# Kernel tuning notes

Measured on AMD Instinct MI355X. Metric: run time of the kernel, lower is better.

## Reference

```python
import jax, jax.numpy as jnp
import numpy as np
import math

V, D, H, FF, L, S, B = 32000, 1024, 16, 4096, 8, 1024, 4
HD = D // H


def _pos_encoding(seq_len, dim):
    pos = np.arange(seq_len)[:, None].astype(np.float32)
    div = np.exp(np.arange(0, dim, 2).astype(np.float32) * -(math.log(10000.0) / dim))
    pe = np.zeros((seq_len, dim), dtype=np.float32)
    pe[:, 0::2] = np.sin(pos * div)
    pe[:, 1::2] = np.cos(pos * div)
    return jnp.asarray(pe)


def setup_inputs() -> dict:
    key = jax.random.key(0)
    ks = jax.random.split(key, 24)
    sc = 0.02
    inp = {
        'tokens': jax.random.randint(ks[0], (B, S), 0, V),
        'emb_W': jax.random.normal(ks[1], (V, D), jnp.float32) * sc,
        'Wq': jax.random.normal(ks[2], (L, D, D), jnp.float32) * sc,
        'bq': jnp.zeros((L, D), jnp.float32),
        'Wk': jax.random.normal(ks[3], (L, D, D), jnp.float32) * sc,
        'bk': jnp.zeros((L, D), jnp.float32),
        'Wv': jax.random.normal(ks[4], (L, D, D), jnp.float32) * sc,
        'bv': jnp.zeros((L, D), jnp.float32),
        'Wo': jax.random.normal(ks[5], (L, D, D), jnp.float32) * sc,
        'bo': jnp.zeros((L, D), jnp.float32),
        'ln1_g': jnp.ones((L, D), jnp.float32),
        'ln1_b': jnp.zeros((L, D), jnp.float32),
        'ln2_g': jnp.ones((L, D), jnp.float32),
        'ln2_b': jnp.zeros((L, D), jnp.float32),
        'W1': jax.random.normal(ks[6], (L, D, FF), jnp.float32) * sc,
        'b1': jnp.zeros((L, FF), jnp.float32),
        'W2': jax.random.normal(ks[7], (L, FF, D), jnp.float32) * sc,
        'b2': jnp.zeros((L, D), jnp.float32),
        'lnf_g': jnp.ones((D,), jnp.float32),
        'lnf_b': jnp.zeros((D,), jnp.float32),
        'head_W': jax.random.normal(ks[8], (D, V), jnp.float32) * sc,
        'head_b': jnp.zeros((V,), jnp.float32),
    }
    return inp


def _layernorm(x, g, b, eps=1e-5):
    mu = jnp.mean(x, axis=-1, keepdims=True)
    var = jnp.mean(jnp.square(x - mu), axis=-1, keepdims=True)
    return (x - mu) * jax.lax.rsqrt(var + eps) * g + b


def _attention(x, Wq, bq, Wk, bk, Wv, bv, Wo, bo, causal_mask):
    b, s, d = x.shape
    q = (x @ Wq + bq).reshape(b, s, H, HD).transpose(0, 2, 1, 3)
    k = (x @ Wk + bk).reshape(b, s, H, HD).transpose(0, 2, 1, 3)
    v = (x @ Wv + bv).reshape(b, s, H, HD).transpose(0, 2, 1, 3)
    scores = jnp.einsum('bhqd,bhkd->bhqk', q, k) / math.sqrt(HD)
    scores = jnp.where(causal_mask, scores, -1e9)
    attn = jax.nn.softmax(scores, axis=-1)
    out = jnp.einsum('bhqk,bhkd->bhqd', attn, v)
    out = out.transpose(0, 2, 1, 3).reshape(b, s, d)
    return out @ Wo + bo


def reference(tokens, emb_W, Wq, bq, Wk, bk, Wv, bv, Wo, bo,
              ln1_g, ln1_b, ln2_g, ln2_b, W1, b1, W2, b2,
              lnf_g, lnf_b, head_W, head_b):
    b, s = tokens.shape
    mask = jnp.tril(jnp.ones((s, s), bool))[None, None]  # (1,1,s,s)
    x = emb_W[tokens] + _pos_encoding(s, D)[None]
    for l in range(L):
        a = _attention(_layernorm(x, ln1_g[l], ln1_b[l]),
                       Wq[l], bq[l], Wk[l], bk[l], Wv[l], bv[l], Wo[l], bo[l], mask)
        x = x + a
        h = _layernorm(x, ln2_g[l], ln2_b[l])
        h = jax.nn.relu(h @ W1[l] + b1[l]) @ W2[l] + b2[l]
        x = x + h
    x = _layernorm(x, lnf_g, lnf_b)
    return x @ head_W + head_b
```

## Files before the change

kernel.cpp:

```cpp
#include <hip/hip_runtime.h>
#include <math.h>


using u16 = unsigned short;
using u32 = unsigned int;
typedef __attribute__((ext_vector_type(4))) float  f32x4;
typedef __attribute__((ext_vector_type(8))) short  s16x8;
typedef __attribute__((ext_vector_type(8))) __bf16 bf16x8;

__device__ __forceinline__ u16 f2bf(float f) {
  u32 u = __builtin_bit_cast(u32, f);
  u += 0x7fffu + ((u >> 16) & 1u);
  return (u16)(u >> 16);
}

__device__ __forceinline__ f32x4 mfma16(s16x8 a, s16x8 b, f32x4 c) {
  return __builtin_amdgcn_mfma_f32_16x16x32_bf16(
      __builtin_bit_cast(bf16x8, a), __builtin_bit_cast(bf16x8, b), c, 0, 0, 0);
}

#define GLD16(gp, lp) __builtin_amdgcn_global_load_lds(                    \
    (const __attribute__((address_space(1))) void*)(gp),                   \
    (__attribute__((address_space(3))) void*)(lp), 16, 0, 0)

__global__ __launch_bounds__(256) void transpose_cvt(
    const float* __restrict__ in, u16* __restrict__ out,
    int C, long long inLS, long long outLS, int outRS)
{
  __shared__ float t[32][33];
  int tr = threadIdx.x >> 5, tc = threadIdx.x & 31;
  const float* ip = in + (size_t)blockIdx.z * inLS +
                    ((size_t)blockIdx.x * 32 + tr) * C + blockIdx.y * 32 + tc;
#pragma unroll
  for (int p = 0; p < 4; ++p) t[p * 8 + tr][tc] = ip[(size_t)p * 8 * C];
  __syncthreads();
  u16* op = out + (size_t)blockIdx.z * outLS +
            ((size_t)blockIdx.y * 32 + tr) * outRS + (size_t)blockIdx.x * 32 + tc;
#pragma unroll
  for (int p = 0; p < 4; ++p) op[(size_t)p * 8 * outRS] = f2bf(t[tc][p * 8 + tr]);
}

__global__ __launch_bounds__(256) void pack_bqkv(
    const float* __restrict__ bq, const float* __restrict__ bk,
    const float* __restrict__ bv, float* __restrict__ outb)
{
  int i = blockIdx.x * 256 + threadIdx.x;
  int ly = i / 3072, j = i % 3072;
  float v = (j < 1024) ? bq[ly * 1024 + j]
          : (j < 2048) ? bk[ly * 1024 + (j - 1024)]
                       : bv[ly * 1024 + (j - 2048)];
  outb[i] = v;
}

__global__ __launch_bounds__(256) void embed_kernel(
    const int* __restrict__ tokens, const float* __restrict__ embW,
    float* __restrict__ x)
{
  int row = blockIdx.x;
  int s = row & 1023;
  int tok = tokens[row];
  int d0 = threadIdx.x * 4;
  float4 e = *(const float4*)&embW[(size_t)tok * 1024 + d0];
  const float c = -9.210340371976184f / 1024.0f;
  float div0 = expf((float)d0 * c);
  float div1 = expf((float)(d0 + 2) * c);
  float sn0, cs0, sn1, cs1;
  sincosf((float)s * div0, &sn0, &cs0);
  sincosf((float)s * div1, &sn1, &cs1);
  float4 r;
  r.x = e.x + sn0; r.y = e.y + cs0; r.z = e.z + sn1; r.w = e.w + cs1;
  *(float4*)&x[(size_t)row * 1024 + d0] = r;
}

__global__ __launch_bounds__(256) void ln_kernel(
    const float* __restrict__ x, const float* __restrict__ g,
    const float* __restrict__ b, u16* __restrict__ y)
{
  int row = blockIdx.x, tid = threadIdx.x;
  float4 v = *(const float4*)&x[(size_t)row * 1024 + tid * 4];
  float sum = v.x + v.y + v.z + v.w;
  float sq = v.x * v.x + v.y * v.y + v.z * v.z + v.w * v.w;
#pragma unroll
  for (int o = 32; o > 0; o >>= 1) {
    sum += __shfl_xor(sum, o, 64);
    sq  += __shfl_xor(sq,  o, 64);
  }
  __shared__ float ps[8];
  int w = tid >> 6;
  if ((tid & 63) == 0) { ps[w] = sum; ps[4 + w] = sq; }
  __syncthreads();
  sum = ps[0] + ps[1] + ps[2] + ps[3];
  sq  = ps[4] + ps[5] + ps[6] + ps[7];
  float mu = sum * (1.0f / 1024.0f);
  float var = sq * (1.0f / 1024.0f) - mu * mu;
  float rs = rsqrtf(var + 1e-5f);
  float4 gg = *(const float4*)&g[tid * 4];
  float4 bb = *(const float4*)&b[tid * 4];
  u32 lo = (u32)f2bf((v.x - mu) * rs * gg.x + bb.x) |
           ((u32)f2bf((v.y - mu) * rs * gg.y + bb.y) << 16);
  u32 hi = (u32)f2bf((v.z - mu) * rs * gg.z + bb.z) |
           ((u32)f2bf((v.w - mu) * rs * gg.w + bb.w) << 16);
  uint2 o2; o2.x = lo; o2.y = hi;
  *(uint2*)&y[(size_t)row * 1024 + tid * 4] = o2;
}

template<int OMODE, int RELU, int NT>
__global__ __launch_bounds__(512, 2) void gemm256(
    const u16* __restrict__ A, const u16* __restrict__ Bt,
    const float* __restrict__ bias, void* Cp, int M, int N, int K, int gx)
{
  __shared__ alignas(16) u16 lds[2][16384];
  const int tid = threadIdx.x;
  const int w = tid >> 6, l = tid & 63;
  const int g = l >> 4, lr = l & 15;
  const int wm = w >> 2, wn = w & 3;
  int nwg = gridDim.x;
  int bid = blockIdx.x;
  int swz = (bid & 7) * (nwg >> 3) + (bid >> 3);
  int bx = swz % gx, by = swz / gx;
  int m0 = by << 8, n0 = bx << 8;

  const u16* Ag[2]; const u16* Bg[2]; int dstE[2];
#pragma unroll
  for (int s2 = 0; s2 < 2; ++s2) {
    int idx = s2 * 512 + tid;
    int row = idx >> 2;
    int ch = (idx & 3) ^ ((row >> 1) & 3);
    Ag[s2] = A  + (size_t)(m0 + row) * K + ch * 8;
    Bg[s2] = Bt + (size_t)(n0 + row) * K + ch * 8;
    dstE[s2] = idx * 8;
  }
  const int colx = (g ^ ((lr >> 1) & 3)) * 8;
  const int aoff = (wm * 128 + lr) * 32 + colx;
  const int boff = 8192 + (wn * 64 + lr) * 32 + colx;

  f32x4 acc[8][4];
#pragma unroll
  for (int i = 0; i < 8; ++i)
#pragma unroll
    for (int j = 0; j < 4; ++j) acc[i][j] = f32x4{0.f, 0.f, 0.f, 0.f};

  const int nk = K >> 5;
#pragma unroll
  for (int s2 = 0; s2 < 2; ++s2) GLD16(Ag[s2], &lds[0][dstE[s2]]);
#pragma unroll
  for (int s2 = 0; s2 < 2; ++s2) GLD16(Bg[s2], &lds[0][8192 + dstE[s2]]);
  asm volatile("s_waitcnt vmcnt(0)" ::: "memory");
  __builtin_amdgcn_s_barrier();

  int cur = 0;
  s16x8 aC[4], aH[4], bC[4];
#pragma unroll
  for (int i = 0; i < 4; ++i) aC[i] = *(const s16x8*)&lds[0][aoff + i * 512];
#pragma unroll
  for (int i = 0; i < 4; ++i) aH[i] = *(const s16x8*)&lds[0][aoff + (4 + i) * 512];
#pragma unroll
  for (int j = 0; j < 4; ++j) bC[j] = *(const s16x8*)&lds[0][boff + j * 512];

  for (int t = 0; t < nk; ++t) {
    const bool more = (t + 1 < nk);
    if (more) {
      const int kn = (t + 1) << 5;
#pragma unroll
      for (int s2 = 0; s2 < 2; ++s2) GLD16(Ag[s2] + kn, &lds[cur ^ 1][dstE[s2]]);
#pragma unroll
      for (int s2 = 0; s2 < 2; ++s2) GLD16(Bg[s2] + kn, &lds[cur ^ 1][8192 + dstE[s2]]);
    }
    __builtin_amdgcn_s_setprio(1);
#pragma unroll
    for (int i = 0; i < 4; ++i)
#pragma unroll
      for (int j = 0; j < 4; ++j) acc[i][j] = mfma16(aC[i], bC[j], acc[i][j]);
#pragma unroll
    for (int i = 0; i < 4; ++i)
#pragma unroll
      for (int j = 0; j < 4; ++j) acc[4 + i][j] = mfma16(aH[i], bC[j], acc[4 + i][j]);
    __builtin_amdgcn_s_setprio(0);
    if (more) {
      asm volatile("s_waitcnt vmcnt(0)" ::: "memory");
      __builtin_amdgcn_s_barrier();
      cur ^= 1;
#pragma unroll
      for (int i = 0; i < 4; ++i) aC[i] = *(const s16x8*)&lds[cur][aoff + i * 512];
#pragma unroll
      for (int i = 0; i < 4; ++i) aH[i] = *(const s16x8*)&lds[cur][aoff + (4 + i) * 512];
#pragma unroll
      for (int j = 0; j < 4; ++j) bC[j] = *(const s16x8*)&lds[cur][boff + j * 512];
    }
  }

  float* fst = (float*)(void*)&lds[0][0];
#pragma unroll
  for (int mf = 0; mf < 8; ++mf) {
    __builtin_amdgcn_s_barrier();
#pragma unroll
    for (int nf = 0; nf < 4; ++nf) {
      int cl = wn * 64 + nf * 16 + lr;
      float bv = bias[n0 + cl];
      int rl = wm * 16 + g * 4;
#pragma unroll
      for (int r = 0; r < 4; ++r) {
        float v = acc[mf][nf][r] + bv;
        if (RELU) v = fmaxf(v, 0.f);
        fst[(rl + r) * 260 + cl] = v;
      }
    }
    __builtin_amdgcn_s_barrier();
    if (OMODE == 0) {
#pragma unroll
      for (int it = 0; it < 2; ++it) {
        int seg = it * 512 + tid;
        int row = seg >> 5;
        int co  = (seg & 31) * 8;
        int grow = m0 + (row >> 4) * 128 + mf * 16 + (row & 15);
        const float* src = &fst[row * 260 + co];
        uint4 q;
        q.x = (u32)f2bf(src[0]) | ((u32)f2bf(src[1]) << 16);
        q.y = (u32)f2bf(src[2]) | ((u32)f2bf(src[3]) << 16);
        q.z = (u32)f2bf(src[4]) | ((u32)f2bf(src[5]) << 16);
        q.w = (u32)f2bf(src[6]) | ((u32)f2bf(src[7]) << 16);
        *(uint4*)&((u16*)Cp)[(size_t)grow * N + n0 + co] = q;
      }
    } else {
#pragma unroll
      for (int it = 0; it < 4; ++it) {
        int seg = it * 512 + tid;
        int row = seg >> 6;
        int co  = (seg & 63) * 4;
        int grow = m0 + (row >> 4) * 128 + mf * 16 + (row & 15);
        f32x4 q = *(const f32x4*)&fst[row * 260 + co];
        float* dp = &((float*)Cp)[(size_t)grow * N + n0 + co];
        if (NT) __builtin_nontemporal_store(q, (f32x4*)dp);
        else    *(f32x4*)dp = q;
      }
    }
  }
}

template<int OMODE, int RELU>
__global__ __launch_bounds__(256, 3) void gemm_p(
    const u16* __restrict__ A, const u16* __restrict__ Bt,
    const float* __restrict__ bias, const float* res, void* Cp,
    int M, int N, int K, int gx)
{
  __shared__ alignas(16) u16 lds[2][8192];
  const int tid = threadIdx.x;
  const int w = tid >> 6, l = tid & 63;
  const int g = l >> 4, lr = l & 15;
  const int wm = w >> 1, wn = w & 1;
  int nwg = gridDim.x;
  int bid = blockIdx.x;
  int swz = (bid & 7) * (nwg >> 3) + (bid >> 3);
  int bx = swz % gx, by = swz / gx;
  int m0 = by << 7, n0 = bx << 7;

  const u16 *Ag[2], *Bg[2];
  int dstA[2], dstB[2];
#pragma unroll
  for (int s = 0; s < 2; ++s) {
    int idx = s * 256 + tid;
    int row = idx >> 2;
    int ch = (idx & 3) ^ ((row >> 1) & 3);
    Ag[s] = A  + (size_t)(m0 + row) * K + ch * 8;
    Bg[s] = Bt + (size_t)(n0 + row) * K + ch * 8;
    dstA[s] = idx * 8;
    dstB[s] = 4096 + idx * 8;
  }
  const int colx = (g ^ ((lr >> 1) & 3)) * 8;
  const int aoff = (wm * 64 + lr) * 32 + colx;
  const int boff = 4096 + (wn * 64 + lr) * 32 + colx;

  f32x4 acc[4][4];
#pragma unroll
  for (int i = 0; i < 4; ++i)
#pragma unroll
    for (int j = 0; j < 4; ++j) acc[i][j] = f32x4{0.f, 0.f, 0.f, 0.f};

  const int nk = K >> 5;
#pragma unroll
  for (int s = 0; s < 2; ++s) GLD16(Ag[s], &lds[0][dstA[s]]);
#pragma unroll
  for (int s = 0; s < 2; ++s) GLD16(Bg[s], &lds[0][dstB[s]]);
  asm volatile("s_waitcnt vmcnt(0)" ::: "memory");
  __builtin_amdgcn_s_barrier();

  int cur = 0;
  s16x8 aC[4], bC[4];
#pragma unroll
  for (int i = 0; i < 4; ++i) aC[i] = *(const s16x8*)&lds[0][aoff + i * 512];
#pragma unroll
  for (int j = 0; j < 4; ++j) bC[j] = *(const s16x8*)&lds[0][boff + j * 512];

  for (int t = 0; t < nk; ++t) {
    const bool more = (t + 1 < nk);
    if (more) {
      const int kn = (t + 1) << 5;
#pragma unroll
      for (int s = 0; s < 2; ++s) GLD16(Ag[s] + kn, &lds[cur ^ 1][dstA[s]]);
#pragma unroll
      for (int s = 0; s < 2; ++s) GLD16(Bg[s] + kn, &lds[cur ^ 1][dstB[s]]);
    }
    __builtin_amdgcn_s_setprio(1);
#pragma unroll
    for (int i = 0; i < 4; ++i)
#pragma unroll
      for (int j = 0; j < 4; ++j) acc[i][j] = mfma16(aC[i], bC[j], acc[i][j]);
    __builtin_amdgcn_s_setprio(0);
    if (more) {
      asm volatile("s_waitcnt vmcnt(0)" ::: "memory");
      __builtin_amdgcn_s_barrier();
      cur ^= 1;
#pragma unroll
      for (int i = 0; i < 4; ++i) aC[i] = *(const s16x8*)&lds[cur][aoff + i * 512];
#pragma unroll
      for (int j = 0; j < 4; ++j) bC[j] = *(const s16x8*)&lds[cur][boff + j * 512];
    }
  }
#pragma unroll
  for (int mf = 0; mf < 4; ++mf) {
    int row = m0 + wm * 64 + mf * 16 + g * 4;
#pragma unroll
    for (int nf = 0; nf < 4; ++nf) {
      int col = n0 + wn * 64 + nf * 16 + lr;
      float bv = bias[col];
#pragma unroll
      for (int r = 0; r < 4; ++r) {
        float v = acc[mf][nf][r] + bv;
        if (RELU) v = fmaxf(v, 0.f);
        size_t idx = (size_t)(row + r) * N + col;
        if (OMODE == 0)      ((u16*)Cp)[idx] = f2bf(v);
        else if (OMODE == 1) ((float*)Cp)[idx] = v + res[idx];
        else                 ((float*)Cp)[idx] = v;
      }
    }
  }
}

__global__ __launch_bounds__(256) void attn_kernel(
    const u16* __restrict__ qkv, u16* __restrict__ outp)
{
  int b = blockIdx.x >> 4, h = blockIdx.x & 15;
  int q0 = blockIdx.y << 6;
  int tid = threadIdx.x, w = tid >> 6, l = tid & 63;
  int g = l >> 4, lr = l & 15;
  const int RS = 3072;
  const u16* base = qkv + (size_t)b * 1024 * RS + h * 64;
  const u16* Qb = base;
  const u16* Kb = base + 1024;
  const u16* Vb = base + 2048;
  __shared__ alignas(16) u16 Plds[4][1024];
  __shared__ alignas(16) u16 Vt[4096];
  char* Pw = (char*)&Plds[w][0];

  s16x8 qf[2];
#pragma unroll
  for (int ks = 0; ks < 2; ++ks)
    qf[ks] = *(const s16x8*)&Qb[(size_t)(q0 + w * 16 + lr) * RS + ks * 32 + g * 8];

  f32x4 o[4];
#pragma unroll
  for (int n = 0; n < 4; ++n) o[n] = f32x4{0.f, 0.f, 0.f, 0.f};
  float mr[4] = {-INFINITY, -INFINITY, -INFINITY, -INFINITY};
  float ls[4] = {0.f, 0.f, 0.f, 0.f};

  int ntile = (q0 >> 6) + 1;
  for (int kt = 0; kt < ntile; ++kt) {
    int kv0 = kt << 6;
    f32x4 sc[4];
#pragma unroll
    for (int t = 0; t < 4; ++t) sc[t] = f32x4{0.f, 0.f, 0.f, 0.f};
#pragma unroll
    for (int ks = 0; ks < 2; ++ks)
#pragma unroll
      for (int t = 0; t < 4; ++t) {
        s16x8 kf = *(const s16x8*)&Kb[(size_t)(kv0 + t * 16 + lr) * RS + ks * 32 + g * 8];
        sc[t] = mfma16(qf[ks], kf, sc[t]);
      }
#pragma unroll
    for (int p = 0; p < 2; ++p) {
      int key = p * 32 + (tid >> 3);
      int d0 = (tid & 7) * 8;
      s16x8 vrow = *(const s16x8*)&Vb[(size_t)(kv0 + key) * RS + d0];
#pragma unroll
      for (int j = 0; j < 8; ++j) {
        int d = d0 + j;
        int byt = (d * 128 + key * 2) ^ ((d & 7) << 4);
        *(u16*)((char*)Vt + byt) = (u16)vrow[j];
      }
    }
    float p4[4][4];
    float tmax[4] = {-INFINITY, -INFINITY, -INFINITY, -INFINITY};
    int qr_base = q0 + w * 16 + g * 4;
#pragma unroll
    for (int t = 0; t < 4; ++t) {
      int key = kv0 + t * 16 + lr;
#pragma unroll
      for (int r = 0; r < 4; ++r) {
        float s = sc[t][r] * 0.125f;
        s = (key <= qr_base + r) ? s : -1e30f;
        p4[t][r] = s;
        tmax[r] = fmaxf(tmax[r], s);
      }
    }
#pragma unroll
    for (int off = 1; off < 16; off <<= 1)
#pragma unroll
      for (int r = 0; r < 4; ++r) tmax[r] = fmaxf(tmax[r], __shfl_xor(tmax[r], off, 64));
    float corr[4], rsum[4];
#pragma unroll
    for (int r = 0; r < 4; ++r) {
      float mn = fmaxf(mr[r], tmax[r]);
      corr[r] = __expf(mr[r] - mn);
      mr[r] = mn;
      rsum[r] = 0.f;
    }
#pragma unroll
    for (int t = 0; t < 4; ++t)
#pragma unroll
      for (int r = 0; r < 4; ++r) {
        float e = __expf(p4[t][r] - mr[r]);
        p4[t][r] = e;
        rsum[r] += e;
      }
#pragma unroll
    for (int off = 1; off < 16; off <<= 1)
#pragma unroll
      for (int r = 0; r < 4; ++r) rsum[r] += __shfl_xor(rsum[r], off, 64);
#pragma unroll
    for (int r = 0; r < 4; ++r) ls[r] = ls[r] * corr[r] + rsum[r];
#pragma unroll
    for (int n = 0; n < 4; ++n)
#pragma unroll
      for (int r = 0; r < 4; ++r) o[n][r] *= corr[r];
#pragma unroll
    for (int t = 0; t < 4; ++t)
#pragma unroll
      for (int r = 0; r < 4; ++r) {
        int prow = g * 4 + r;
        int byt = (prow * 128 + (t * 16 + lr) * 2) ^ ((prow & 7) << 4);
        *(u16*)(Pw + byt) = f2bf(p4[t][r]);
      }
    __syncthreads();
#pragma unroll
    for (int ks = 0; ks < 2; ++ks) {
      int ab = (lr * 128 + ks * 64 + g * 16) ^ ((lr & 7) << 4);
      s16x8 pa = *(const s16x8*)(Pw + ab);
#pragma unroll
      for (int n = 0; n < 4; ++n) {
        int vb2 = ((n * 16 + lr) * 128 + ks * 64 + g * 16) ^ ((lr & 7) << 4);
        s16x8 vfr = *(const s16x8*)((const char*)Vt + vb2);
        o[n] = mfma16(pa, vfr, o[n]);
      }
    }
    __syncthreads();
  }
#pragma unroll
  for (int n = 0; n < 4; ++n)
#pragma unroll
    for (int r = 0; r < 4; ++r) {
      float v = o[n][r] / ls[r];
      outp[(size_t)(b * 1024 + q0 + w * 16 + g * 4 + r) * 1024 + h * 64 + n * 16 + lr] = f2bf(v);
    }
}

extern "C" void kernel_launch(void* const* d_in, const int* in_sizes, int n_in,
                              void* d_out, int out_size, void* d_ws, size_t ws_size,
                              hipStream_t stream)
{
  const int*   tokens = (const int*)  d_in[0];
  const float* embW   = (const float*)d_in[1];
  const float* Wq     = (const float*)d_in[2];
  const float* bq     = (const float*)d_in[3];
  const float* Wk     = (const float*)d_in[4];
  const float* bk     = (const float*)d_in[5];
  const float* Wv     = (const float*)d_in[6];
  const float* bv     = (const float*)d_in[7];
  const float* Wo     = (const float*)d_in[8];
  const float* bo     = (const float*)d_in[9];
  const float* ln1g   = (const float*)d_in[10];
  const float* ln1b   = (const float*)d_in[11];
  const float* ln2g   = (const float*)d_in[12];
  const float* ln2b   = (const float*)d_in[13];
  const float* W1     = (const float*)d_in[14];
  const float* b1     = (const float*)d_in[15];
  const float* W2     = (const float*)d_in[16];
  const float* b2     = (const float*)d_in[17];
  const float* lnfg   = (const float*)d_in[18];
  const float* lnfb   = (const float*)d_in[19];
  const float* headW  = (const float*)d_in[20];
  const float* headb  = (const float*)d_in[21];
  (void)in_sizes; (void)n_in; (void)out_size;

  char* ws = (char*)d_ws;
  u16*   qkvT = (u16*)(ws);
  u16*   woT  = (u16*)(ws + 50331648);
  u16*   w1T  = (u16*)(ws + 67108864);
  u16*   w2T  = (u16*)(ws + 134217728);
  u16*   headT= (u16*)(ws + 201326592);
  float* bqkv = (float*)(ws + 266862592);
  float* x    = (float*)(ws + 266960896);
  u16*   y    = (u16*)(ws + 283738112);
  u16*   qkv  = (u16*)(ws + 292126720);
  u16*   attno= (u16*)(ws + 317292544);
  u16*   h1   = (u16*)(ws + 325681152);
  if (ws_size < 359235584ull) return;

  dim3 blk(256);
  dim3 blk5(512);
  transpose_cvt<<<dim3(32, 32, 8),  blk, 0, stream>>>(Wq, qkvT,           1024,  1048576LL, 3145728LL, 1024);
  transpose_cvt<<<dim3(32, 32, 8),  blk, 0, stream>>>(Wk, qkvT + 1048576, 1024,  1048576LL, 3145728LL, 1024);
  transpose_cvt<<<dim3(32, 32, 8),  blk, 0, stream>>>(Wv, qkvT + 2097152, 1024,  1048576LL, 3145728LL, 1024);
  transpose_cvt<<<dim3(32, 32, 8),  blk, 0, stream>>>(Wo, woT,            1024,  1048576LL, 1048576LL, 1024);
  transpose_cvt<<<dim3(32, 128, 8), blk, 0, stream>>>(W1, w1T,            4096,  4194304LL, 4194304LL, 1024);
  transpose_cvt<<<dim3(128, 32, 8), blk, 0, stream>>>(W2, w2T,            1024,  4194304LL, 4194304LL, 4096);
  transpose_cvt<<<dim3(32, 1000, 1),blk, 0, stream>>>(headW, headT,       32000, 0LL,       0LL,       1024);
  pack_bqkv<<<96, blk, 0, stream>>>(bq, bk, bv, bqkv);
  embed_kernel<<<4096, blk, 0, stream>>>(tokens, embW, x);
  for (int ly = 0; ly < 8; ++ly) {
    ln_kernel<<<4096, blk, 0, stream>>>(x, ln1g + ly * 1024, ln1b + ly * 1024, y);
    gemm256<0, 0, 0><<<192, blk5, 0, stream>>>(y, qkvT + (size_t)ly * 3145728,
        bqkv + ly * 3072, qkv, 4096, 3072, 1024, 12);
    attn_kernel<<<dim3(64, 16), blk, 0, stream>>>(qkv, attno);
    gemm_p<1, 0><<<256, blk, 0, stream>>>(attno, woT + (size_t)ly * 1048576,
        bo + ly * 1024, x, x, 4096, 1024, 1024, 8);
    ln_kernel<<<4096, blk, 0, stream>>>(x, ln2g + ly * 1024, ln2b + ly * 1024, y);
    gemm256<0, 1, 0><<<256, blk5, 0, stream>>>(y, w1T + (size_t)ly * 4194304,
        b1 + ly * 4096, h1, 4096, 4096, 1024, 16);
    gemm_p<1, 0><<<256, blk, 0, stream>>>(h1, w2T + (size_t)ly * 4194304,
        b2 + ly * 1024, x, x, 4096, 1024, 4096, 8);
  }
  ln_kernel<<<4096, blk, 0, stream>>>(x, lnfg, lnfb, y);
  gemm256<2, 0, 1><<<2000, blk5, 0, stream>>>(y, headT, headb,
      (float*)d_out, 4096, 32000, 1024, 125);
}
```

Before: 2.776 ms.

## Double GEMM K-tile to 64, re-swizzle LDS, add M-major tile ordering for head

The 256x256 GEMM now stages 64-wide K slices, using an 8-chunk XOR swizzle, and loads all fragments from LDS at the start of each iteration. This halves the number of barriers per K. A template flag selects M-major block ordering, which the LM-head GEMM uses so that weight tiles get reused across M. Nontemporal stores are removed. The LDS footprint doubles to 128KB, which likely limits residency to one block per CU and removes the register prefetch overlap.

```diff
diff --git a/kernel.cpp b/kernel.cpp
--- a/kernel.cpp
+++ b/kernel.cpp
@@ -104,12 +104,12 @@
   *(uint2*)&y[(size_t)row * 1024 + tid * 4] = o2;
 }
 
-template<int OMODE, int RELU, int NT>
+template<int OMODE, int RELU, int BYMAJ>
 __global__ __launch_bounds__(512, 2) void gemm256(
     const u16* __restrict__ A, const u16* __restrict__ Bt,
-    const float* __restrict__ bias, void* Cp, int M, int N, int K, int gx)
-{
-  __shared__ alignas(16) u16 lds[2][16384];
+    const float* __restrict__ bias, void* Cp, int M, int N, int K, int gd)
+{
+  __shared__ alignas(16) u16 lds[2][32768];
   const int tid = threadIdx.x;
   const int w = tid >> 6, l = tid & 63;
   const int g = l >> 4, lr = l & 15;
@@ -117,22 +117,25 @@
   int nwg = gridDim.x;
   int bid = blockIdx.x;
   int swz = (bid & 7) * (nwg >> 3) + (bid >> 3);
-  int bx = swz % gx, by = swz / gx;
+  int bx, by;
+  if (BYMAJ) { by = swz % gd; bx = swz / gd; }
+  else       { bx = swz % gd; by = swz / gd; }
   int m0 = by << 8, n0 = bx << 8;
 
-  const u16* Ag[2]; const u16* Bg[2]; int dstE[2];
-#pragma unroll
-  for (int s2 = 0; s2 < 2; ++s2) {
+  const u16* Ag[4]; const u16* Bg[4]; int dstE[4];
+#pragma unroll
+  for (int s2 = 0; s2 < 4; ++s2) {
     int idx = s2 * 512 + tid;
-    int row = idx >> 2;
-    int ch = (idx & 3) ^ ((row >> 1) & 3);
+    int row = idx >> 3;
+    int ch = (idx & 7) ^ (row & 7);
     Ag[s2] = A  + (size_t)(m0 + row) * K + ch * 8;
     Bg[s2] = Bt + (size_t)(n0 + row) * K + ch * 8;
     dstE[s2] = idx * 8;
   }
-  const int colx = (g ^ ((lr >> 1) & 3)) * 8;
-  const int aoff = (wm * 128 + lr) * 32 + colx;
-  const int boff = 8192 + (wn * 64 + lr) * 32 + colx;
+  const int colx0 = ((g)     ^ (lr & 7)) * 8;
+  const int colx1 = ((4 + g) ^ (lr & 7)) * 8;
+  const int abase = (wm * 128 + lr) * 64;
+  const int bbase = 16384 + (wn * 64 + lr) * 64;
 
   f32x4 acc[8][4];
 #pragma unroll
@@ -140,52 +143,47 @@
 #pragma unroll
     for (int j = 0; j < 4; ++j) acc[i][j] = f32x4{0.f, 0.f, 0.f, 0.f};
 
-  const int nk = K >> 5;
-#pragma unroll
-  for (int s2 = 0; s2 < 2; ++s2) GLD16(Ag[s2], &lds[0][dstE[s2]]);
-#pragma unroll
-  for (int s2 = 0; s2 < 2; ++s2) GLD16(Bg[s2], &lds[0][8192 + dstE[s2]]);
+  const int nk = K >> 6;
+#pragma unroll
+  for (int s2 = 0; s2 < 4; ++s2) GLD16(Ag[s2], &lds[0][dstE[s2]]);
+#pragma unroll
+  for (int s2 = 0; s2 < 4; ++s2) GLD16(Bg[s2], &lds[0][16384 + dstE[s2]]);
   asm volatile("s_waitcnt vmcnt(0)" ::: "memory");
   __builtin_amdgcn_s_barrier();
 
   int cur = 0;
-  s16x8 aC[4], aH[4], bC[4];
-#pragma unroll
-  for (int i = 0; i < 4; ++i) aC[i] = *(const s16x8*)&lds[0][aoff + i * 512];
-#pragma unroll
-  for (int i = 0; i < 4; ++i) aH[i] = *(const s16x8*)&lds[0][aoff + (4 + i) * 512];
-#pragma unroll
-  for (int j = 0; j < 4; ++j) bC[j] = *(const s16x8*)&lds[0][boff + j * 512];
-
   for (int t = 0; t < nk; ++t) {
     const bool more = (t + 1 < nk);
     if (more) {
-      const int kn = (t + 1) << 5;
-#pragma unroll
-      for (int s2 = 0; s2 < 2; ++s2) GLD16(Ag[s2] + kn, &lds[cur ^ 1][dstE[s2]]);
-#pragma unroll
-      for (int s2 = 0; s2 < 2; ++s2) GLD16(Bg[s2] + kn, &lds[cur ^ 1][8192 + dstE[s2]]);
-    }
+      const int kn = (t + 1) << 6;
+#pragma unroll
+      for (int s2 = 0; s2 < 4; ++s2) GLD16(Ag[s2] + kn, &lds[cur ^ 1][dstE[s2]]);
+#pragma unroll
+      for (int s2 = 0; s2 < 4; ++s2) GLD16(Bg[s2] + kn, &lds[cur ^ 1][16384 + dstE[s2]]);
+    }
+    s16x8 a0[8], b0[4], a1[8], b1[4];
+#pragma unroll
+    for (int mf = 0; mf < 8; ++mf) a0[mf] = *(const s16x8*)&lds[cur][abase + mf * 1024 + colx0];
+#pragma unroll
+    for (int nf = 0; nf < 4; ++nf) b0[nf] = *(const s16x8*)&lds[cur][bbase + nf * 1024 + colx0];
+#pragma unroll
+    for (int mf = 0; mf < 8; ++mf) a1[mf] = *(const s16x8*)&lds[cur][abase + mf * 1024 + colx1];
+#pragma unroll
+    for (int nf = 0; nf < 4; ++nf) b1[nf] = *(const s16x8*)&lds[cur][bbase + nf * 1024 + colx1];
     __builtin_amdgcn_s_setprio(1);
 #pragma unroll
-    for (int i = 0; i < 4; ++i)
-#pragma unroll
-      for (int j = 0; j < 4; ++j) acc[i][j] = mfma16(aC[i], bC[j], acc[i][j]);
-#pragma unroll
-    for (int i = 0; i < 4; ++i)
-#pragma unroll
-      for (int j = 0; j < 4; ++j) acc[4 + i][j] = mfma16(aH[i], bC[j], acc[4 + i][j]);
+    for (int mf = 0; mf < 8; ++mf)
+#pragma unroll
+      for (int nf = 0; nf < 4; ++nf) acc[mf][nf] = mfma16(a0[mf], b0[nf], acc[mf][nf]);
+#pragma unroll
+    for (int mf = 0; mf < 8; ++mf)
+#pragma unroll
+      for (int nf = 0; nf < 4; ++nf) acc[mf][nf] = mfma16(a1[mf], b1[nf], acc[mf][nf]);
     __builtin_amdgcn_s_setprio(0);
     if (more) {
       asm volatile("s_waitcnt vmcnt(0)" ::: "memory");
       __builtin_amdgcn_s_barrier();
       cur ^= 1;
-#pragma unroll
-      for (int i = 0; i < 4; ++i) aC[i] = *(const s16x8*)&lds[cur][aoff + i * 512];
-#pragma unroll
-      for (int i = 0; i < 4; ++i) aH[i] = *(const s16x8*)&lds[cur][aoff + (4 + i) * 512];
-#pragma unroll
-      for (int j = 0; j < 4; ++j) bC[j] = *(const s16x8*)&lds[cur][boff + j * 512];
     }
   }
 
@@ -229,9 +227,7 @@
         int co  = (seg & 63) * 4;
         int grow = m0 + (row >> 4) * 128 + mf * 16 + (row & 15);
         f32x4 q = *(const f32x4*)&fst[row * 260 + co];
-        float* dp = &((float*)Cp)[(size_t)grow * N + n0 + co];
-        if (NT) __builtin_nontemporal_store(q, (f32x4*)dp);
-        else    *(f32x4*)dp = q;
+        *(f32x4*)&((float*)Cp)[(size_t)grow * N + n0 + co] = q;
       }
     }
   }
@@ -531,5 +527,5 @@
   }
   ln_kernel<<<4096, blk, 0, stream>>>(x, lnfg, lnfb, y);
   gemm256<2, 0, 1><<<2000, blk5, 0, stream>>>(y, headT, headb,
-      (float*)d_out, 4096, 32000, 1024, 125);
-}
+      (float*)d_out, 4096, 32000, 1024, 16);
+}
```

New measurement: 2.681 ms. 1.04x faster.
